# Kernel tuning notes

Hardware: AMD Instinct MI355X
Metric: run time of the kernel (lower is better)

The kernel has to match this reference:

```python
import jax, jax.numpy as jnp
import numpy as np

N_USER = 100000
N_ITEM = 100000
N_NODES = N_USER + N_ITEM
NNZ = 6400000
EMB = 64
BATCH = 1024
EPS = 1e-12


def setup_inputs() -> dict:
    key = jax.random.key(0)
    ks = jax.random.split(key, 24)
    inp = {
        'users': jax.random.randint(ks[0], (BATCH,), 0, N_USER, dtype=jnp.int32),
        'pos_items': jax.random.randint(ks[1], (BATCH,), 0, N_ITEM, dtype=jnp.int32),
        'neg_items': jax.random.randint(ks[2], (BATCH,), 0, N_ITEM, dtype=jnp.int32),
        'adj_row': jnp.sort(jax.random.randint(ks[3], (NNZ,), 0, N_NODES, dtype=jnp.int32)),
        'adj_col': jax.random.randint(ks[4], (NNZ,), 0, N_NODES, dtype=jnp.int32),
        # normalized adjacency values are small positive numbers
        'adj_val': jax.random.uniform(ks[5], (NNZ,), dtype=jnp.float32) * 0.05,
        'user_emb': jax.random.normal(ks[6], (N_USER, EMB), dtype=jnp.float32) * 0.1,
        'item_emb': jax.random.normal(ks[7], (N_ITEM, EMB), dtype=jnp.float32) * 0.1,
    }
    i = 8
    for k in range(3):
        inp[f'W_gc_{k}'] = jax.random.normal(ks[i], (EMB, EMB), dtype=jnp.float32) * (1.0 / np.sqrt(EMB)); i += 1
        inp[f'b_gc_{k}'] = jax.random.normal(ks[i], (1, EMB), dtype=jnp.float32) * 0.01; i += 1
        inp[f'W_bi_{k}'] = jax.random.normal(ks[i], (EMB, EMB), dtype=jnp.float32) * (1.0 / np.sqrt(EMB)); i += 1
        inp[f'b_bi_{k}'] = jax.random.normal(ks[i], (1, EMB), dtype=jnp.float32) * 0.01; i += 1
    return inp


def _spmm(row, col, val, x):
    # A_hat @ x  for COO sparse A_hat of shape [N_NODES, N_NODES]
    gathered = val[:, None] * x[col]           # [nnz, d]
    return jax.ops.segment_sum(gathered, row, num_segments=N_NODES)


def _l2norm(x):
    # F.normalize(x, p=2, dim=1) with eps clamp
    n = jnp.sqrt(jnp.sum(x * x, axis=1, keepdims=True))
    return x / jnp.maximum(n, EPS)


def reference(users, pos_items, neg_items, adj_row, adj_col, adj_val,
              user_emb, item_emb,
              W_gc_0, b_gc_0, W_bi_0, b_bi_0,
              W_gc_1, b_gc_1, W_bi_1, b_bi_1,
              W_gc_2, b_gc_2, W_bi_2, b_bi_2):
    Wgc = [W_gc_0, W_gc_1, W_gc_2]
    bgc = [b_gc_0, b_gc_1, b_gc_2]
    Wbi = [W_bi_0, W_bi_1, W_bi_2]
    bbi = [b_bi_0, b_bi_1, b_bi_2]

    ego = jnp.concatenate([user_emb, item_emb], axis=0)   # [N, 64]
    all_embeddings = [ego]
    for k in range(3):
        side = _spmm(adj_row, adj_col, adj_val, ego)       # SpMM aggregation
        sum_emb = side @ Wgc[k] + bgc[k]
        bi_emb = (ego * side) @ Wbi[k] + bbi[k]
        ego = jax.nn.leaky_relu(sum_emb + bi_emb, negative_slope=0.2)
        # mess dropout skipped (eval / deterministic baseline)
        all_embeddings.append(_l2norm(ego))
    all_emb = jnp.concatenate(all_embeddings, axis=1)      # [N, 256]

    u_g = all_emb[:N_USER]
    i_g = all_emb[N_USER:]
    return (u_g[users], i_g[pos_items], i_g[neg_items])
```

## Files before the change

kernel.cpp:

```cpp
#include <hip/hip_runtime.h>

#define N_USER 100000
#define N_ITEM 100000
#define N_NODES 200000
#define NNZ 6400000
#define EMB 64
#define BATCH 1024
#define B3 (3 * BATCH)

typedef __attribute__((ext_vector_type(8))) short bf16x8;
typedef __attribute__((ext_vector_type(4))) float f32x4;


__device__ __forceinline__ unsigned short f2bf(float f) {
    unsigned int b = __builtin_bit_cast(unsigned int, f);
    b += 0x7FFFu + ((b >> 16) & 1u);
    return (unsigned short)(b >> 16);
}
__device__ __forceinline__ float bf2f(unsigned short u) {
    return __builtin_bit_cast(float, (unsigned int)u << 16);
}
__device__ __forceinline__ unsigned int pack2(float lo, float hi) {
    return ((unsigned int)f2bf(hi) << 16) | f2bf(lo);
}

__device__ __forceinline__ bf16x8 mul_bf(bf16x8 a, bf16x8 b) {
    bf16x8 r;
#pragma unroll
    for (int j = 0; j < 8; ++j) {
        float f = bf2f((unsigned short)a[j]) * bf2f((unsigned short)b[j]);
        r[j] = (short)f2bf(f);
    }
    return r;
}

__global__ void build_row_ptr(const int* __restrict__ row, int* __restrict__ row_ptr) {
    int i = blockIdx.x * blockDim.x + threadIdx.x;
    if (i >= NNZ) return;
    int b = row[i];
    int a = (i == 0) ? -1 : row[i - 1];
    for (int r = a + 1; r <= b; ++r) row_ptr[r] = i;
    if (i == NNZ - 1) {
        for (int r = b + 1; r <= N_NODES; ++r) row_ptr[r] = NNZ;
    }
}

__global__ void concat_ego(const float* __restrict__ ue, const float* __restrict__ ie,
                           unsigned short* __restrict__ ego_h) {
    int i = blockIdx.x * blockDim.x + threadIdx.x;
    const int nu4 = N_USER * EMB / 4;
    const int tot4 = N_NODES * EMB / 4;
    if (i >= tot4) return;
    float4 v = (i < nu4) ? ((const float4*)ue)[i] : ((const float4*)ie)[i - nu4];
    uint2 o;
    o.x = pack2(v.x, v.y);
    o.y = pack2(v.z, v.w);
    ((uint2*)ego_h)[i] = o;
}

__global__ void prep_wfrags(const float* __restrict__ W0, const float* __restrict__ W1,
                            const float* __restrict__ W2, const float* __restrict__ W3,
                            const float* __restrict__ W4, const float* __restrict__ W5,
                            unsigned short* __restrict__ wfrag) {
    int m = blockIdx.x >> 3;
    int t = (blockIdx.x >> 1) & 3, c = blockIdx.x & 1;
    const float* W = m == 0 ? W0 : m == 1 ? W1 : m == 2 ? W2 : m == 3 ? W3 : m == 4 ? W4 : W5;
    int l = threadIdx.x, quad = l >> 4, n = l & 15;
    unsigned short* dst = wfrag + ((size_t)blockIdx.x * 64 + l) * 8;
#pragma unroll
    for (int j = 0; j < 8; ++j)
        dst[j] = f2bf(W[(c * 32 + quad * 8 + j) * 64 + t * 16 + n]);
}

__device__ __forceinline__ int batch_node(const int* users, const int* pos,
                                          const int* neg, int b) {
    int t = b >> 10, idx = b & 1023;
    if (t == 0) return users[idx];
    if (t == 1) return N_USER + pos[idx];
    return N_USER + neg[idx];
}

__global__ void gather_layer0(const int* __restrict__ users, const int* __restrict__ pos,
                              const int* __restrict__ neg, const float* __restrict__ ue,
                              const float* __restrict__ ie, float* __restrict__ out) {
    int b = blockIdx.x;
    int node = batch_node(users, pos, neg, b);
    float v = (node < N_USER) ? ue[(size_t)node * EMB + threadIdx.x]
                              : ie[(size_t)(node - N_USER) * EMB + threadIdx.x];
    out[(size_t)b * 256 + threadIdx.x] = v;
}


__global__ void zero_flags(int* __restrict__ flags) {
    int i = blockIdx.x * blockDim.x + threadIdx.x;
    if (i < N_NODES + 4) flags[i] = 0;
}

__global__ __launch_bounds__(256) void build_frontier(
        const int* __restrict__ users, const int* __restrict__ pos,
        const int* __restrict__ neg, const int* __restrict__ row_ptr,
        const int* __restrict__ col, int* __restrict__ flags,
        int* __restrict__ list2, int* __restrict__ cnt) {
    int w = (blockIdx.x * blockDim.x + threadIdx.x) >> 6;
    int lane = threadIdx.x & 63;
    if (w >= B3) return;
    int node = batch_node(users, pos, neg, w);
    if (lane == 0) {
        if (atomicOr(&flags[node], 1) == 0) list2[atomicAdd(cnt, 1)] = node;
    }
    int j0 = row_ptr[node], j1 = row_ptr[node + 1];
    for (int j = j0 + lane; j < j1; j += 64) {
        int c = col[j];
        if (atomicOr(&flags[c], 1) == 0) list2[atomicAdd(cnt, 1)] = c;
    }
}


__device__ __forceinline__ void spmm_row(
        int row, int lane, const int* __restrict__ row_ptr,
        const int* __restrict__ col, const float* __restrict__ val,
        const unsigned short* __restrict__ xh, unsigned short* __restrict__ dst) {
    int q = lane >> 4, p = lane & 15;
    int q4 = q << 2;
    unsigned p4 = (unsigned)p * 4u;
    int j0 = row_ptr[row], j1 = row_ptr[row + 1];
    float a0 = 0.f, a1 = 0.f, a2 = 0.f, a3 = 0.f;
    for (int j = j0; j < j1; j += 32) {
        int jl = j + (lane & 31);
        bool ok = jl < j1;
        int cc = ok ? __builtin_nontemporal_load(col + jl) : 0;
        int vv = ok ? __builtin_bit_cast(int, __builtin_nontemporal_load(val + jl))
                    : 0;
        int n = j1 - j;
#pragma unroll
        for (int g = 0; g < 4; ++g) {
            if (g * 8 >= n) break;
#pragma unroll
            for (int s = 0; s < 2; ++s) {
                const int t = g * 8 + s * 4;
                int   ct = __builtin_amdgcn_ds_bpermute(q4 + t * 4, cc);
                float vt = __builtin_bit_cast(float,
                            __builtin_amdgcn_ds_bpermute(q4 + t * 4, vv));
                unsigned idx = (unsigned)ct * 64u + p4;
                uint2 d = *(const uint2*)(xh + idx);
                float f0 = __builtin_bit_cast(float, d.x << 16);
                float f1 = __builtin_bit_cast(float, d.x & 0xffff0000u);
                float f2 = __builtin_bit_cast(float, d.y << 16);
                float f3 = __builtin_bit_cast(float, d.y & 0xffff0000u);
                a0 = fmaf(vt, f0, a0);
                a1 = fmaf(vt, f1, a1);
                a2 = fmaf(vt, f2, a2);
                a3 = fmaf(vt, f3, a3);
            }
        }
    }
    a0 += __shfl_xor(a0, 16); a0 += __shfl_xor(a0, 32);
    a1 += __shfl_xor(a1, 16); a1 += __shfl_xor(a1, 32);
    a2 += __shfl_xor(a2, 16); a2 += __shfl_xor(a2, 32);
    a3 += __shfl_xor(a3, 16); a3 += __shfl_xor(a3, 32);
    if (q == 0) {
        uint2 o;
        o.x = pack2(a0, a1);
        o.y = pack2(a2, a3);
        ((uint2*)dst)[p] = o;
    }
}

__global__ __launch_bounds__(256) void spmm_full(
        const int* __restrict__ row_ptr, const int* __restrict__ col,
        const float* __restrict__ val, const unsigned short* __restrict__ xh,
        unsigned short* __restrict__ yh) {
    int wave = (blockIdx.x * blockDim.x + threadIdx.x) >> 6;
    if (wave >= N_NODES) return;
    spmm_row(wave, threadIdx.x & 63, row_ptr, col, val, xh, yh + (size_t)wave * EMB);
}

__global__ __launch_bounds__(256) void spmm_list(
        const int* __restrict__ row_ptr, const int* __restrict__ col,
        const float* __restrict__ val, const unsigned short* __restrict__ xh,
        unsigned short* __restrict__ yh, const int* __restrict__ list,
        const int* __restrict__ cntp) {
    int wave = (blockIdx.x * blockDim.x + threadIdx.x) >> 6;
    if (wave >= *cntp) return;
    int row = list[wave];
    spmm_row(row, threadIdx.x & 63, row_ptr, col, val, xh, yh + (size_t)row * EMB);
}

__global__ __launch_bounds__(256) void spmm_batch(
        const int* __restrict__ row_ptr, const int* __restrict__ col,
        const float* __restrict__ val, const unsigned short* __restrict__ xh,
        unsigned short* __restrict__ side3, const int* __restrict__ users,
        const int* __restrict__ pos, const int* __restrict__ neg) {
    int wave = (blockIdx.x * blockDim.x + threadIdx.x) >> 6;
    if (wave >= B3) return;
    int row = batch_node(users, pos, neg, wave);
    spmm_row(row, threadIdx.x & 63, row_ptr, col, val, xh, side3 + (size_t)wave * EMB);
}


__device__ __forceinline__ void dense_core(
        const unsigned short* __restrict__ aside,
        const unsigned short* __restrict__ aego,
        const unsigned short* __restrict__ wf, int lane,
        const float* __restrict__ bgc, const float* __restrict__ bbi,
        f32x4 acc[4]) {
    int quad = lane >> 4, n = lane & 15;

    bf16x8 bfrag[2][4][2];
#pragma unroll
    for (int m = 0; m < 2; ++m)
#pragma unroll
        for (int t = 0; t < 4; ++t)
#pragma unroll
            for (int c = 0; c < 2; ++c)
                bfrag[m][t][c] = *(const bf16x8*)(wf + ((size_t)((m * 4 + t) * 2 + c) * 64 + lane) * 8);

#pragma unroll
    for (int t = 0; t < 4; ++t) {
        float bs = bgc[t * 16 + n] + bbi[t * 16 + n];
        acc[t] = (f32x4){bs, bs, bs, bs};
    }

    bf16x8 as0 = *(const bf16x8*)(aside + quad * 8);
    bf16x8 as1 = *(const bf16x8*)(aside + quad * 8 + 32);
    bf16x8 ae0 = *(const bf16x8*)(aego + quad * 8);
    bf16x8 ae1 = *(const bf16x8*)(aego + quad * 8 + 32);
    bf16x8 ap0 = mul_bf(ae0, as0);
    bf16x8 ap1 = mul_bf(ae1, as1);

#pragma unroll
    for (int t = 0; t < 4; ++t) {
        acc[t] = __builtin_amdgcn_mfma_f32_16x16x32_bf16(as0, bfrag[0][t][0], acc[t], 0, 0, 0);
        acc[t] = __builtin_amdgcn_mfma_f32_16x16x32_bf16(as1, bfrag[0][t][1], acc[t], 0, 0, 0);
        acc[t] = __builtin_amdgcn_mfma_f32_16x16x32_bf16(ap0, bfrag[1][t][0], acc[t], 0, 0, 0);
        acc[t] = __builtin_amdgcn_mfma_f32_16x16x32_bf16(ap1, bfrag[1][t][1], acc[t], 0, 0, 0);
    }
}

__global__ __launch_bounds__(256) void dense_mfma(
        const unsigned short* __restrict__ side_h,
        unsigned short* __restrict__ ego_h,
        const unsigned short* __restrict__ wf,
        const float* __restrict__ bgc, const float* __restrict__ bbi,
        const int* __restrict__ list, const int* __restrict__ cntp) {
    int wave = threadIdx.x >> 6;
    int lane = threadIdx.x & 63;
    int quad = lane >> 4, n = lane & 15;
    int base = (blockIdx.x * 4 + wave) * 16;
    int cntv = list ? *cntp : N_NODES;
    if (base >= cntv) return;

    int rA = base + n;
    if (list) rA = list[rA < cntv ? rA : cntv - 1];

    f32x4 acc[4];
    dense_core(side_h + (size_t)rA * EMB, ego_h + (size_t)rA * EMB,
               wf, lane, bgc, bbi, acc);

    int rw[4];
#pragma unroll
    for (int i = 0; i < 4; ++i) {
        int r = base + quad * 4 + i;
        rw[i] = (r < cntv) ? (list ? list[r] : r) : -1;
    }
#pragma unroll
    for (int t = 0; t < 4; ++t)
#pragma unroll
        for (int i = 0; i < 4; ++i) {
            if (rw[i] < 0) continue;
            float v = acc[t][i];
            float o = v > 0.f ? v : 0.2f * v;
            ego_h[(size_t)rw[i] * EMB + t * 16 + n] = f2bf(o);
        }
}

__global__ __launch_bounds__(256) void dense_batch(
        const unsigned short* __restrict__ side3,
        const unsigned short* __restrict__ ego_h,
        const int* __restrict__ users, const int* __restrict__ pos,
        const int* __restrict__ neg, const unsigned short* __restrict__ wf,
        const float* __restrict__ bgc, const float* __restrict__ bbi,
        float* __restrict__ ego3) {
    int wave = threadIdx.x >> 6;
    int lane = threadIdx.x & 63;
    int quad = lane >> 4, n = lane & 15;
    int b0 = blockIdx.x * 64 + wave * 16;
    int bA = b0 + n;
    int nodeA = batch_node(users, pos, neg, bA);

    f32x4 acc[4];
    dense_core(side3 + (size_t)bA * EMB, ego_h + (size_t)nodeA * EMB,
               wf, lane, bgc, bbi, acc);

#pragma unroll
    for (int t = 0; t < 4; ++t)
#pragma unroll
        for (int i = 0; i < 4; ++i) {
            float v = acc[t][i];
            float o = v > 0.f ? v : 0.2f * v;
            ego3[(size_t)(b0 + quad * 4 + i) * EMB + t * 16 + n] = o;
        }
}

__global__ void gather_norm(const int* __restrict__ users, const int* __restrict__ pos,
                            const int* __restrict__ neg,
                            const unsigned short* __restrict__ ego_h,
                            float* __restrict__ out, int layer) {
    int b = blockIdx.x;
    int lane = threadIdx.x;
    int node = batch_node(users, pos, neg, b);
    float v = bf2f(ego_h[(size_t)node * EMB + lane]);
    float s = v * v;
#pragma unroll
    for (int off = 32; off > 0; off >>= 1) s += __shfl_xor(s, off);
    float n = fmaxf(sqrtf(s), 1e-12f);
    out[(size_t)b * 256 + layer * EMB + lane] = v / n;
}

__global__ void gather_norm_b3(const float* __restrict__ ego3, float* __restrict__ out) {
    int b = blockIdx.x;
    int lane = threadIdx.x;
    float v = ego3[(size_t)b * EMB + lane];
    float s = v * v;
#pragma unroll
    for (int off = 32; off > 0; off >>= 1) s += __shfl_xor(s, off);
    float n = fmaxf(sqrtf(s), 1e-12f);
    out[(size_t)b * 256 + 192 + lane] = v / n;
}

extern "C" void kernel_launch(void* const* d_in, const int* in_sizes, int n_in,
                              void* d_out, int out_size, void* d_ws, size_t ws_size,
                              hipStream_t stream) {
    const int*   users    = (const int*)d_in[0];
    const int*   pos      = (const int*)d_in[1];
    const int*   neg      = (const int*)d_in[2];
    const int*   adj_row  = (const int*)d_in[3];
    const int*   adj_col  = (const int*)d_in[4];
    const float* adj_val  = (const float*)d_in[5];
    const float* user_emb = (const float*)d_in[6];
    const float* item_emb = (const float*)d_in[7];

    unsigned short* ego_h   = (unsigned short*)d_ws;
    unsigned short* side_h  = ego_h + (size_t)N_NODES * EMB;
    int*            row_ptr = (int*)(side_h + (size_t)N_NODES * EMB);
    unsigned short* wfrag   = (unsigned short*)(row_ptr + 200704);
    int*            flags   = (int*)(wfrag + 6 * 8 * 64 * 8);
    int*            cnt     = flags + N_NODES;
    int*            list2   = cnt + 4;
    unsigned short* side3   = (unsigned short*)(list2 + N_NODES);
    float*          ego3    = (float*)(side3 + (size_t)B3 * EMB);
    float*          out     = (float*)d_out;

    build_row_ptr<<<(NNZ + 255) / 256, 256, 0, stream>>>(adj_row, row_ptr);
    concat_ego<<<(N_NODES * EMB / 4 + 255) / 256, 256, 0, stream>>>(user_emb, item_emb, ego_h);
    prep_wfrags<<<48, 64, 0, stream>>>((const float*)d_in[8], (const float*)d_in[10],
                                       (const float*)d_in[12], (const float*)d_in[14],
                                       (const float*)d_in[16], (const float*)d_in[18], wfrag);
    gather_layer0<<<B3, 64, 0, stream>>>(users, pos, neg, user_emb, item_emb, out);

    zero_flags<<<(N_NODES + 4 + 255) / 256, 256, 0, stream>>>(flags);
    build_frontier<<<B3 / 4, 256, 0, stream>>>(users, pos, neg, row_ptr, adj_col,
                                               flags, list2, cnt);

    {
        const float* bgc = (const float*)d_in[9];
        const float* bbi = (const float*)d_in[11];
        spmm_full<<<N_NODES / 4, 256, 0, stream>>>(row_ptr, adj_col, adj_val, ego_h, side_h);
        dense_mfma<<<N_NODES / 64, 256, 0, stream>>>(side_h, ego_h, wfrag, bgc, bbi,
                                                     nullptr, nullptr);
        gather_norm<<<B3, 64, 0, stream>>>(users, pos, neg, ego_h, out, 1);
    }
    {
        const float* bgc = (const float*)d_in[13];
        const float* bbi = (const float*)d_in[15];
        spmm_list<<<N_NODES / 4, 256, 0, stream>>>(row_ptr, adj_col, adj_val, ego_h,
                                                   side_h, list2, cnt);
        dense_mfma<<<N_NODES / 64, 256, 0, stream>>>(side_h, ego_h,
                                                     wfrag + (size_t)1 * 2 * 8 * 64 * 8,
                                                     bgc, bbi, list2, cnt);
        gather_norm<<<B3, 64, 0, stream>>>(users, pos, neg, ego_h, out, 2);
    }
    {
        const float* bgc = (const float*)d_in[17];
        const float* bbi = (const float*)d_in[19];
        spmm_batch<<<B3 / 4, 256, 0, stream>>>(row_ptr, adj_col, adj_val, ego_h,
                                               side3, users, pos, neg);
        dense_batch<<<B3 / 64, 256, 0, stream>>>(side3, ego_h, users, pos, neg,
                                                 wfrag + (size_t)2 * 2 * 8 * 64 * 8,
                                                 bgc, bbi, ego3);
        gather_norm_b3<<<B3, 64, 0, stream>>>(ego3, out);
    }
}
```

Before: 488.0 us.

## Fuse setup, frontier, norm and layer-3 kernels to cut launch count

Merges the setup kernels (row_ptr build, ego concat, weight fragment prep, layer-0 gather, flag zeroing) into one block-partitioned launch. The frontier build now rides in extra blocks of the full SpMM, and the layer-1 and layer-2 gather-norms run in extra blocks of the following SpMM and layer-3 kernels. Layer 3 computes its SpMM rows into shared memory, does the dense MFMA and L2-normalises in one kernel, which removes the side3/ego3 round trips. The intent is fewer launches and less global traffic for small batch-sized stages. The cost is more branchy kernels and, in layer 3, serial per-wave SpMM over 16 rows before a sync.

```diff
diff --git a/kernel.cpp b/kernel.cpp
--- a/kernel.cpp
+++ b/kernel.cpp
@@ -34,44 +34,6 @@
     return r;
 }
 
-__global__ void build_row_ptr(const int* __restrict__ row, int* __restrict__ row_ptr) {
-    int i = blockIdx.x * blockDim.x + threadIdx.x;
-    if (i >= NNZ) return;
-    int b = row[i];
-    int a = (i == 0) ? -1 : row[i - 1];
-    for (int r = a + 1; r <= b; ++r) row_ptr[r] = i;
-    if (i == NNZ - 1) {
-        for (int r = b + 1; r <= N_NODES; ++r) row_ptr[r] = NNZ;
-    }
-}
-
-__global__ void concat_ego(const float* __restrict__ ue, const float* __restrict__ ie,
-                           unsigned short* __restrict__ ego_h) {
-    int i = blockIdx.x * blockDim.x + threadIdx.x;
-    const int nu4 = N_USER * EMB / 4;
-    const int tot4 = N_NODES * EMB / 4;
-    if (i >= tot4) return;
-    float4 v = (i < nu4) ? ((const float4*)ue)[i] : ((const float4*)ie)[i - nu4];
-    uint2 o;
-    o.x = pack2(v.x, v.y);
-    o.y = pack2(v.z, v.w);
-    ((uint2*)ego_h)[i] = o;
-}
-
-__global__ void prep_wfrags(const float* __restrict__ W0, const float* __restrict__ W1,
-                            const float* __restrict__ W2, const float* __restrict__ W3,
-                            const float* __restrict__ W4, const float* __restrict__ W5,
-                            unsigned short* __restrict__ wfrag) {
-    int m = blockIdx.x >> 3;
-    int t = (blockIdx.x >> 1) & 3, c = blockIdx.x & 1;
-    const float* W = m == 0 ? W0 : m == 1 ? W1 : m == 2 ? W2 : m == 3 ? W3 : m == 4 ? W4 : W5;
-    int l = threadIdx.x, quad = l >> 4, n = l & 15;
-    unsigned short* dst = wfrag + ((size_t)blockIdx.x * 64 + l) * 8;
-#pragma unroll
-    for (int j = 0; j < 8; ++j)
-        dst[j] = f2bf(W[(c * 32 + quad * 8 + j) * 64 + t * 16 + n]);
-}
-
 __device__ __forceinline__ int batch_node(const int* users, const int* pos,
                                           const int* neg, int b) {
     int t = b >> 10, idx = b & 1023;
@@ -80,46 +42,84 @@
     return N_USER + neg[idx];
 }
 
-__global__ void gather_layer0(const int* __restrict__ users, const int* __restrict__ pos,
-                              const int* __restrict__ neg, const float* __restrict__ ue,
-                              const float* __restrict__ ie, float* __restrict__ out) {
-    int b = blockIdx.x;
-    int node = batch_node(users, pos, neg, b);
-    float v = (node < N_USER) ? ue[(size_t)node * EMB + threadIdx.x]
-                              : ie[(size_t)(node - N_USER) * EMB + threadIdx.x];
-    out[(size_t)b * 256 + threadIdx.x] = v;
-}
-
-
-__global__ void zero_flags(int* __restrict__ flags) {
-    int i = blockIdx.x * blockDim.x + threadIdx.x;
-    if (i < N_NODES + 4) flags[i] = 0;
-}
-
-__global__ __launch_bounds__(256) void build_frontier(
+#define SB_ROWPTR 25000
+#define SB_CONCAT 12800
+#define SB_WFRAG  12
+#define SB_GATH0  768
+#define SB_ZFLAG  784
+#define SETUP_BLOCKS (SB_ROWPTR + SB_CONCAT + SB_WFRAG + SB_GATH0 + SB_ZFLAG)
+
+__global__ __launch_bounds__(256) void setup_fused(
+        const int* __restrict__ row, const float* __restrict__ ue,
+        const float* __restrict__ ie,
+        const float* __restrict__ W0, const float* __restrict__ W1,
+        const float* __restrict__ W2, const float* __restrict__ W3,
+        const float* __restrict__ W4, const float* __restrict__ W5,
         const int* __restrict__ users, const int* __restrict__ pos,
-        const int* __restrict__ neg, const int* __restrict__ row_ptr,
-        const int* __restrict__ col, int* __restrict__ flags,
-        int* __restrict__ list2, int* __restrict__ cnt) {
-    int w = (blockIdx.x * blockDim.x + threadIdx.x) >> 6;
-    int lane = threadIdx.x & 63;
-    if (w >= B3) return;
-    int node = batch_node(users, pos, neg, w);
-    if (lane == 0) {
-        if (atomicOr(&flags[node], 1) == 0) list2[atomicAdd(cnt, 1)] = node;
-    }
-    int j0 = row_ptr[node], j1 = row_ptr[node + 1];
-    for (int j = j0 + lane; j < j1; j += 64) {
-        int c = col[j];
-        if (atomicOr(&flags[c], 1) == 0) list2[atomicAdd(cnt, 1)] = c;
-    }
-}
-
+        const int* __restrict__ neg,
+        int* __restrict__ row_ptr, unsigned short* __restrict__ ego_h,
+        unsigned short* __restrict__ wfrag, float* __restrict__ out,
+        int* __restrict__ flags) {
+    unsigned bx = blockIdx.x;
+    int tx = threadIdx.x;
+    if (bx < SB_ROWPTR) {
+        int i = bx * 256 + tx;
+        int b = row[i];
+        int a = (i == 0) ? -1 : row[i - 1];
+        for (int r = a + 1; r <= b; ++r) row_ptr[r] = i;
+        if (i == NNZ - 1)
+            for (int r = b + 1; r <= N_NODES; ++r) row_ptr[r] = NNZ;
+        return;
+    }
+    bx -= SB_ROWPTR;
+    if (bx < SB_CONCAT) {
+        int i = bx * 256 + tx;
+        const int nu4 = N_USER * EMB / 4;
+        const int tot4 = N_NODES * EMB / 4;
+        if (i < tot4) {
+            float4 v = (i < nu4) ? ((const float4*)ue)[i] : ((const float4*)ie)[i - nu4];
+            uint2 o;
+            o.x = pack2(v.x, v.y);
+            o.y = pack2(v.z, v.w);
+            ((uint2*)ego_h)[i] = o;
+        }
+        return;
+    }
+    bx -= SB_CONCAT;
+    if (bx < SB_WFRAG) {
+        int ob = bx * 4 + (tx >> 6);
+        int l = tx & 63;
+        int m = ob >> 3, t = (ob >> 1) & 3, c = ob & 1;
+        const float* W = m == 0 ? W0 : m == 1 ? W1 : m == 2 ? W2
+                       : m == 3 ? W3 : m == 4 ? W4 : W5;
+        int quad = l >> 4, n = l & 15;
+        unsigned short* dst = wfrag + ((size_t)ob * 64 + l) * 8;
+#pragma unroll
+        for (int j = 0; j < 8; ++j)
+            dst[j] = f2bf(W[(c * 32 + quad * 8 + j) * 64 + t * 16 + n]);
+        return;
+    }
+    bx -= SB_WFRAG;
+    if (bx < SB_GATH0) {
+        int b = bx * 4 + (tx >> 6);
+        int lane = tx & 63;
+        int node = batch_node(users, pos, neg, b);
+        float v = (node < N_USER) ? ue[(size_t)node * EMB + lane]
+                                  : ie[(size_t)(node - N_USER) * EMB + lane];
+        out[(size_t)b * 256 + lane] = v;
+        return;
+    }
+    bx -= SB_GATH0;
+    {
+        int i = bx * 256 + tx;
+        if (i < N_NODES + 4) flags[i] = 0;
+    }
+}
 
 __device__ __forceinline__ void spmm_row(
         int row, int lane, const int* __restrict__ row_ptr,
         const int* __restrict__ col, const float* __restrict__ val,
-        const unsigned short* __restrict__ xh, unsigned short* __restrict__ dst) {
+        const unsigned short* __restrict__ xh, unsigned short* dst) {
     int q = lane >> 4, p = lane & 15;
     int q4 = q << 2;
     unsigned p4 = (unsigned)p * 4u;
@@ -166,41 +166,59 @@
     }
 }
 
-__global__ __launch_bounds__(256) void spmm_full(
+#define SPMM_BLOCKS (N_NODES / 4)
+
+__global__ __launch_bounds__(256) void spmm_full_frontier(
         const int* __restrict__ row_ptr, const int* __restrict__ col,
         const float* __restrict__ val, const unsigned short* __restrict__ xh,
-        unsigned short* __restrict__ yh) {
-    int wave = (blockIdx.x * blockDim.x + threadIdx.x) >> 6;
-    if (wave >= N_NODES) return;
-    spmm_row(wave, threadIdx.x & 63, row_ptr, col, val, xh, yh + (size_t)wave * EMB);
-}
-
-__global__ __launch_bounds__(256) void spmm_list(
+        unsigned short* __restrict__ yh, const int* __restrict__ users,
+        const int* __restrict__ pos, const int* __restrict__ neg,
+        int* __restrict__ flags, int* __restrict__ list2, int* __restrict__ cnt) {
+    int lane = threadIdx.x & 63;
+    if (blockIdx.x < SPMM_BLOCKS) {
+        int wave = (blockIdx.x * 256 + threadIdx.x) >> 6;
+        spmm_row(wave, lane, row_ptr, col, val, xh, yh + (size_t)wave * EMB);
+        return;
+    }
+    int w = (blockIdx.x - SPMM_BLOCKS) * 4 + (threadIdx.x >> 6);
+    int node = batch_node(users, pos, neg, w);
+    if (lane == 0) {
+        if (atomicOr(&flags[node], 1) == 0) list2[atomicAdd(cnt, 1)] = node;
+    }
+    int j0 = row_ptr[node], j1 = row_ptr[node + 1];
+    for (int j = j0 + lane; j < j1; j += 64) {
+        int c = col[j];
+        if (atomicOr(&flags[c], 1) == 0) list2[atomicAdd(cnt, 1)] = c;
+    }
+}
+
+__global__ __launch_bounds__(256) void spmm_list_norm1(
         const int* __restrict__ row_ptr, const int* __restrict__ col,
         const float* __restrict__ val, const unsigned short* __restrict__ xh,
         unsigned short* __restrict__ yh, const int* __restrict__ list,
-        const int* __restrict__ cntp) {
-    int wave = (blockIdx.x * blockDim.x + threadIdx.x) >> 6;
-    if (wave >= *cntp) return;
-    int row = list[wave];
-    spmm_row(row, threadIdx.x & 63, row_ptr, col, val, xh, yh + (size_t)row * EMB);
-}
-
-__global__ __launch_bounds__(256) void spmm_batch(
-        const int* __restrict__ row_ptr, const int* __restrict__ col,
-        const float* __restrict__ val, const unsigned short* __restrict__ xh,
-        unsigned short* __restrict__ side3, const int* __restrict__ users,
-        const int* __restrict__ pos, const int* __restrict__ neg) {
-    int wave = (blockIdx.x * blockDim.x + threadIdx.x) >> 6;
-    if (wave >= B3) return;
-    int row = batch_node(users, pos, neg, wave);
-    spmm_row(row, threadIdx.x & 63, row_ptr, col, val, xh, side3 + (size_t)wave * EMB);
-}
-
+        const int* __restrict__ cntp, const int* __restrict__ users,
+        const int* __restrict__ pos, const int* __restrict__ neg,
+        float* __restrict__ out) {
+    int lane = threadIdx.x & 63;
+    if (blockIdx.x < SPMM_BLOCKS) {
+        int wave = (blockIdx.x * 256 + threadIdx.x) >> 6;
+        if (wave >= *cntp) return;
+        int row = list[wave];
+        spmm_row(row, lane, row_ptr, col, val, xh, yh + (size_t)row * EMB);
+        return;
+    }
+    int b = (blockIdx.x - SPMM_BLOCKS) * 4 + (threadIdx.x >> 6);
+    int node = batch_node(users, pos, neg, b);
+    float v = bf2f(xh[(size_t)node * EMB + lane]);
+    float s = v * v;
+#pragma unroll
+    for (int off = 32; off > 0; off >>= 1) s += __shfl_xor(s, off);
+    float nn = fmaxf(sqrtf(s), 1e-12f);
+    out[(size_t)b * 256 + 1 * EMB + lane] = v / nn;
+}
 
 __device__ __forceinline__ void dense_core(
-        const unsigned short* __restrict__ aside,
-        const unsigned short* __restrict__ aego,
+        const unsigned short* aside, const unsigned short* aego,
         const unsigned short* __restrict__ wf, int lane,
         const float* __restrict__ bgc, const float* __restrict__ bbi,
         f32x4 acc[4]) {
@@ -274,58 +292,60 @@
         }
 }
 
-__global__ __launch_bounds__(256) void dense_batch(
-        const unsigned short* __restrict__ side3,
-        const unsigned short* __restrict__ ego_h,
+#define L3_BLOCKS (B3 / 64)
+__global__ __launch_bounds__(256) void layer3_norm2(
+        const int* __restrict__ row_ptr, const int* __restrict__ col,
+        const float* __restrict__ val, const unsigned short* __restrict__ ego_h,
         const int* __restrict__ users, const int* __restrict__ pos,
         const int* __restrict__ neg, const unsigned short* __restrict__ wf,
         const float* __restrict__ bgc, const float* __restrict__ bbi,
-        float* __restrict__ ego3) {
+        float* __restrict__ out) {
+    __shared__ unsigned short sside[64 * 72];
+    int lane = threadIdx.x & 63;
+    if (blockIdx.x >= L3_BLOCKS) {
+        int b = (blockIdx.x - L3_BLOCKS) * 4 + (threadIdx.x >> 6);
+        int node = batch_node(users, pos, neg, b);
+        float v = bf2f(ego_h[(size_t)node * EMB + lane]);
+        float s = v * v;
+#pragma unroll
+        for (int off = 32; off > 0; off >>= 1) s += __shfl_xor(s, off);
+        float nn = fmaxf(sqrtf(s), 1e-12f);
+        out[(size_t)b * 256 + 2 * EMB + lane] = v / nn;
+        return;
+    }
     int wave = threadIdx.x >> 6;
-    int lane = threadIdx.x & 63;
+    int b0 = blockIdx.x * 64;
+    for (int r = 0; r < 16; ++r) {
+        int bpos = b0 + wave * 16 + r;
+        int node = batch_node(users, pos, neg, bpos);
+        spmm_row(node, lane, row_ptr, col, val, ego_h, &sside[(wave * 16 + r) * 72]);
+    }
+    __syncthreads();
     int quad = lane >> 4, n = lane & 15;
-    int b0 = blockIdx.x * 64 + wave * 16;
-    int bA = b0 + n;
-    int nodeA = batch_node(users, pos, neg, bA);
-
+    int nodeA = batch_node(users, pos, neg, b0 + wave * 16 + n);
     f32x4 acc[4];
-    dense_core(side3 + (size_t)bA * EMB, ego_h + (size_t)nodeA * EMB,
+    dense_core(&sside[(wave * 16 + n) * 72], ego_h + (size_t)nodeA * EMB,
                wf, lane, bgc, bbi, acc);
-
+    float ov[4][4];
 #pragma unroll
     for (int t = 0; t < 4; ++t)
 #pragma unroll
         for (int i = 0; i < 4; ++i) {
             float v = acc[t][i];
-            float o = v > 0.f ? v : 0.2f * v;
-            ego3[(size_t)(b0 + quad * 4 + i) * EMB + t * 16 + n] = o;
+            ov[t][i] = v > 0.f ? v : 0.2f * v;
         }
-}
-
-__global__ void gather_norm(const int* __restrict__ users, const int* __restrict__ pos,
-                            const int* __restrict__ neg,
-                            const unsigned short* __restrict__ ego_h,
-                            float* __restrict__ out, int layer) {
-    int b = blockIdx.x;
-    int lane = threadIdx.x;
-    int node = batch_node(users, pos, neg, b);
-    float v = bf2f(ego_h[(size_t)node * EMB + lane]);
-    float s = v * v;
-#pragma unroll
-    for (int off = 32; off > 0; off >>= 1) s += __shfl_xor(s, off);
-    float n = fmaxf(sqrtf(s), 1e-12f);
-    out[(size_t)b * 256 + layer * EMB + lane] = v / n;
-}
-
-__global__ void gather_norm_b3(const float* __restrict__ ego3, float* __restrict__ out) {
-    int b = blockIdx.x;
-    int lane = threadIdx.x;
-    float v = ego3[(size_t)b * EMB + lane];
-    float s = v * v;
-#pragma unroll
-    for (int off = 32; off > 0; off >>= 1) s += __shfl_xor(s, off);
-    float n = fmaxf(sqrtf(s), 1e-12f);
-    out[(size_t)b * 256 + 192 + lane] = v / n;
+#pragma unroll
+    for (int i = 0; i < 4; ++i) {
+        float s = ov[0][i] * ov[0][i] + ov[1][i] * ov[1][i]
+                + ov[2][i] * ov[2][i] + ov[3][i] * ov[3][i];
+        s += __shfl_xor(s, 1); s += __shfl_xor(s, 2);
+        s += __shfl_xor(s, 4); s += __shfl_xor(s, 8);
+        float ninv = 1.f / fmaxf(sqrtf(s), 1e-12f);
+        int bpos = b0 + wave * 16 + quad * 4 + i;
+#pragma unroll
+        for (int t = 0; t < 4; ++t)
+            out[(size_t)bpos * 256 + 192 + t * 16 + n] = ov[t][i] * ninv;
+    }
 }
 
 extern "C" void kernel_launch(void* const* d_in, const int* in_sizes, int n_in,
@@ -347,47 +367,32 @@
     int*            flags   = (int*)(wfrag + 6 * 8 * 64 * 8);
     int*            cnt     = flags + N_NODES;
     int*            list2   = cnt + 4;
-    unsigned short* side3   = (unsigned short*)(list2 + N_NODES);
-    float*          ego3    = (float*)(side3 + (size_t)B3 * EMB);
     float*          out     = (float*)d_out;
 
-    build_row_ptr<<<(NNZ + 255) / 256, 256, 0, stream>>>(adj_row, row_ptr);
-    concat_ego<<<(N_NODES * EMB / 4 + 255) / 256, 256, 0, stream>>>(user_emb, item_emb, ego_h);
-    prep_wfrags<<<48, 64, 0, stream>>>((const float*)d_in[8], (const float*)d_in[10],
-                                       (const float*)d_in[12], (const float*)d_in[14],
-                                       (const float*)d_in[16], (const float*)d_in[18], wfrag);
-    gather_layer0<<<B3, 64, 0, stream>>>(users, pos, neg, user_emb, item_emb, out);
-
-    zero_flags<<<(N_NODES + 4 + 255) / 256, 256, 0, stream>>>(flags);
-    build_frontier<<<B3 / 4, 256, 0, stream>>>(users, pos, neg, row_ptr, adj_col,
-                                               flags, list2, cnt);
-
-    {
-        const float* bgc = (const float*)d_in[9];
-        const float* bbi = (const float*)d_in[11];
-        spmm_full<<<N_NODES / 4, 256, 0, stream>>>(row_ptr, adj_col, adj_val, ego_h, side_h);
-        dense_mfma<<<N_NODES / 64, 256, 0, stream>>>(side_h, ego_h, wfrag, bgc, bbi,
-                                                     nullptr, nullptr);
-        gather_norm<<<B3, 64, 0, stream>>>(users, pos, neg, ego_h, out, 1);
-    }
-    {
-        const float* bgc = (const float*)d_in[13];
-        const float* bbi = (const float*)d_in[15];
-        spmm_list<<<N_NODES / 4, 256, 0, stream>>>(row_ptr, adj_col, adj_val, ego_h,
-                                                   side_h, list2, cnt);
-        dense_mfma<<<N_NODES / 64, 256, 0, stream>>>(side_h, ego_h,
-                                                     wfrag + (size_t)1 * 2 * 8 * 64 * 8,
-                                                     bgc, bbi, list2, cnt);
-        gather_norm<<<B3, 64, 0, stream>>>(users, pos, neg, ego_h, out, 2);
-    }
-    {
-        const float* bgc = (const float*)d_in[17];
-        const float* bbi = (const float*)d_in[19];
-        spmm_batch<<<B3 / 4, 256, 0, stream>>>(row_ptr, adj_col, adj_val, ego_h,
-                                               side3, users, pos, neg);
-        dense_batch<<<B3 / 64, 256, 0, stream>>>(side3, ego_h, users, pos, neg,
-                                                 wfrag + (size_t)2 * 2 * 8 * 64 * 8,
-                                                 bgc, bbi, ego3);
-        gather_norm_b3<<<B3, 64, 0, stream>>>(ego3, out);
-    }
-}
+    setup_fused<<<SETUP_BLOCKS, 256, 0, stream>>>(
+        adj_row, user_emb, item_emb,
+        (const float*)d_in[8],  (const float*)d_in[10], (const float*)d_in[12],
+        (const float*)d_in[14], (const float*)d_in[16], (const float*)d_in[18],
+        users, pos, neg, row_ptr, ego_h, wfrag, out, flags);
+
+    spmm_full_frontier<<<SPMM_BLOCKS + B3 / 4, 256, 0, stream>>>(
+        row_ptr, adj_col, adj_val, ego_h, side_h, users, pos, neg,
+        flags, list2, cnt);
+
+    dense_mfma<<<N_NODES / 64, 256, 0, stream>>>(
+        side_h, ego_h, wfrag, (const float*)d_in[9], (const float*)d_in[11],
+        nullptr, nullptr);
+
+    spmm_list_norm1<<<SPMM_BLOCKS + B3 / 4, 256, 0, stream>>>(
+        row_ptr, adj_col, adj_val, ego_h, side_h, list2, cnt,
+        users, pos, neg, out);
+
+    dense_mfma<<<N_NODES / 64, 256, 0, stream>>>(
+        side_h, ego_h, wfrag + (size_t)1 * 2 * 8 * 64 * 8,
+        (const float*)d_in[13], (const float*)d_in[15], list2, cnt);
+
+    layer3_norm2<<<L3_BLOCKS + B3 / 4, 256, 0, stream>>>(
+        row_ptr, adj_col, adj_val, ego_h, users, pos, neg,
+        wfrag + (size_t)2 * 2 * 8 * 64 * 8,
+        (const float*)d_in[17], (const float*)d_in[19], out);
+}
```

After: 509.7 us. +4.4%, slower.
